# Kernel optimization log

Measured on AMD Instinct MI355X. Metric: run time of the kernel, lower is better.

## Reference

```python
import jax, jax.numpy as jnp
import numpy as np

H, KVH, D, BS, L = 32, 8, 128, 16, 4096
MAX_BLOCKS = L // BS          # 256 blocks per sequence (sink cache capacity)
B = 16
NUM_BLOCKS = B * MAX_BLOCKS   # 4096 total cache blocks
T = MAX_BLOCKS * BS           # 4096 linearized cache slots per sequence
SCALE = 1.0 / np.sqrt(D)


def _rope_cos_sin(pos):
    # neox-style RoPE tables; pos: int array [...]. returns cos/sin [..., D/2]
    inv_freq = 1.0 / (10000.0 ** (jnp.arange(0, D, 2, dtype=jnp.float32) / D))
    ang = pos[..., None].astype(jnp.float32) * inv_freq
    return jnp.cos(ang), jnp.sin(ang)


def _apply_rope(x, cos, sin):
    # x [..., D]; cos/sin broadcastable to x[..., :D//2]
    x1, x2 = jnp.split(x, 2, axis=-1)
    return jnp.concatenate([x1 * cos - x2 * sin, x2 * cos + x1 * sin], axis=-1)


def setup_inputs() -> dict:
    key = jax.random.key(0)
    ks = jax.random.split(key, 6)
    q = jax.random.normal(ks[0], (B, H * D), dtype=jnp.float32)
    k = jax.random.normal(ks[1], (B, KVH * D), dtype=jnp.float32)
    v = jax.random.normal(ks[2], (B, KVH * D), dtype=jnp.float32)
    key_cache = jax.random.normal(ks[3], (NUM_BLOCKS, BS, KVH, D), dtype=jnp.float32)
    value_cache = jax.random.normal(ks[4], (NUM_BLOCKS, BS, KVH, D), dtype=jnp.float32)
    block_tables = jnp.arange(B * MAX_BLOCKS, dtype=jnp.int32).reshape(B, MAX_BLOCKS)
    context_lens = jax.random.randint(ks[5], (B,), 0, 6000, dtype=jnp.int32)
    return {"q": q, "k": k, "v": v, "key_cache": key_cache,
            "value_cache": value_cache, "block_tables": block_tables,
            "context_lens": context_lens}


def reference(q, k, v, key_cache, value_cache, block_tables, context_lens):
    ctx = context_lens.astype(jnp.int32)                         # [B] past tokens
    rem = ctx % BS
    # sink/rolling cap: if past >= model_context_len, effective seq len caps
    seq_len = jnp.where(ctx >= L, L - BS + rem + 1, ctx + 1)     # [B]
    pos_q = seq_len - 1                                          # capped current position

    # gather pre-rope keys/values from paged cache -> [B, T, KVH, D]
    keys = key_cache[block_tables].reshape(B, T, KVH, D)
    vals = value_cache[block_tables].reshape(B, T, KVH, D)

    # re-apply rope to gathered keys at their cache-relative positions 0..T-1
    cos_k, sin_k = _rope_cos_sin(jnp.arange(T))                  # [T, D/2]
    keys = _apply_rope(keys, cos_k[None, :, None, :], sin_k[None, :, None, :])

    # rope current q, k at capped positions
    cos_q, sin_q = _rope_cos_sin(pos_q)                          # [B, D/2]
    qh = _apply_rope(q.reshape(B, H, D), cos_q[:, None, :], sin_q[:, None, :])
    kh = _apply_rope(k.reshape(B, KVH, D), cos_q[:, None, :], sin_q[:, None, :])

    # scatter current token's k/v at its slot (offset rem in last used block == seq_len-1)
    bidx = jnp.arange(B)
    keys = keys.at[bidx, pos_q].set(kh)
    vals = vals.at[bidx, pos_q].set(v.reshape(B, KVH, D))

    # GQA attention over first seq_len cached tokens
    G = H // KVH
    qg = qh.reshape(B, KVH, G, D)
    scores = jnp.einsum('bhgd,bthd->bhgt', qg, keys) * SCALE     # [B, KVH, G, T]
    mask = jnp.arange(T)[None, :] < seq_len[:, None]             # [B, T]
    scores = jnp.where(mask[:, None, None, :], scores, jnp.finfo(scores.dtype).min)
    probs = jax.nn.softmax(scores, axis=-1)
    out = jnp.einsum('bhgt,bthd->bhgd', probs, vals)             # [B, KVH, G, D]
    return out.reshape(B, H * D)
```

## Files before the change

kernel.cpp:

```cpp
#include <hip/hip_runtime.h>
#include <math.h>

#define B_      16
#define H_      32
#define KVH_    8
#define G_      4
#define D_      128
#define BS_     16
#define L_      4096
#define MAXB_   256
#define T_      4096
#define NPART_  8
#define PART_   512
#define SCALE_  0.08838834764831843f

__device__ __forceinline__ int seq_len_of(int ctx) {
  return (ctx >= L_) ? (L_ - BS_ + (ctx & (BS_ - 1)) + 1) : (ctx + 1);
}

__global__ void rope_table_kernel(float* __restrict__ tab) {
  int idx = blockIdx.x * blockDim.x + threadIdx.x;
  if (idx >= T_ * 64) return;
  int t = idx >> 6, i = idx & 63;
  double inv = pow(10000.0, -(double)(2 * i) / 128.0);
  float ang = (float)t * (float)inv;
  double a = (double)ang;
  tab[2 * idx]     = (float)cos(a);
  tab[2 * idx + 1] = (float)sin(a);
}

__global__ __launch_bounds__(256) void attn_partial_kernel(
    const float* __restrict__ q, const float* __restrict__ knew,
    const float* __restrict__ vnew, const float* __restrict__ kc,
    const float* __restrict__ vc, const int* __restrict__ btab,
    const int* __restrict__ ctxl, const float* __restrict__ tab,
    float* __restrict__ opart, float2* __restrict__ ml) {
  int bid  = blockIdx.x;
  int part = bid & (NPART_ - 1);
  int kvh  = (bid >> 3) & (KVH_ - 1);
  int b    = bid >> 6;

  int seq = seq_len_of(ctxl[b]);
  int t0 = part * PART_;
  if (t0 >= seq) return;
  int t1 = min(t0 + PART_, seq);
  int posq = seq - 1;

  int lane = threadIdx.x & 63;
  int wave = threadIdx.x >> 6;
  int tsub = lane >> 4;
  int dg   = lane & 15;

  const float4* tab4 = (const float4*)tab;
  float4 cq0 = tab4[posq * 32 + 2 * dg];
  float4 cq1 = tab4[posq * 32 + 2 * dg + 1];

  float q1[G_][4], q2[G_][4];
#pragma unroll
  for (int g = 0; g < G_; ++g) {
    const float* qp = q + b * (H_ * D_) + (kvh * G_ + g) * D_;
    float4 a  = *(const float4*)(qp + 4 * dg);
    float4 bq = *(const float4*)(qp + 64 + 4 * dg);
    q1[g][0] = (a.x * cq0.x - bq.x * cq0.y) * SCALE_;
    q2[g][0] = (bq.x * cq0.x + a.x * cq0.y) * SCALE_;
    q1[g][1] = (a.y * cq0.z - bq.y * cq0.w) * SCALE_;
    q2[g][1] = (bq.y * cq0.z + a.y * cq0.w) * SCALE_;
    q1[g][2] = (a.z * cq1.x - bq.z * cq1.y) * SCALE_;
    q2[g][2] = (bq.z * cq1.x + a.z * cq1.y) * SCALE_;
    q1[g][3] = (a.w * cq1.z - bq.w * cq1.w) * SCALE_;
    q2[g][3] = (bq.w * cq1.z + a.w * cq1.w) * SCALE_;
  }

  float kn1[4], kn2[4];
  float4 vna, vnb;
  {
    const float* kp = knew + b * (KVH_ * D_) + kvh * D_;
    float4 a  = *(const float4*)(kp + 4 * dg);
    float4 bq = *(const float4*)(kp + 64 + 4 * dg);
    kn1[0] = a.x * cq0.x - bq.x * cq0.y;  kn2[0] = bq.x * cq0.x + a.x * cq0.y;
    kn1[1] = a.y * cq0.z - bq.y * cq0.w;  kn2[1] = bq.y * cq0.z + a.y * cq0.w;
    kn1[2] = a.z * cq1.x - bq.z * cq1.y;  kn2[2] = bq.z * cq1.x + a.z * cq1.y;
    kn1[3] = a.w * cq1.z - bq.w * cq1.w;  kn2[3] = bq.w * cq1.z + a.w * cq1.w;
    const float* vp = vnew + b * (KVH_ * D_) + kvh * D_;
    vna = *(const float4*)(vp + 4 * dg);
    vnb = *(const float4*)(vp + 64 + 4 * dg);
  }

  float m[G_], l[G_], acc[G_][8];
#pragma unroll
  for (int g = 0; g < G_; ++g) {
    m[g] = -1e30f; l[g] = 0.f;
#pragma unroll
    for (int j = 0; j < 8; ++j) acc[g][j] = 0.f;
  }

  for (int tq = t0 + 4 * wave; tq < t1; tq += 16) {
    int t = tq + tsub;
    if (t < t1) {
      int blk  = btab[b * MAXB_ + (t >> 4)];
      int base = ((blk * BS_ + (t & (BS_ - 1))) * KVH_ + kvh) * D_;
      const float4* kc4 = (const float4*)(kc + base);
      const float4* vc4 = (const float4*)(vc + base);
      float4 ka = kc4[dg],      kb = kc4[16 + dg];
      float4 va = vc4[dg],      vb = vc4[16 + dg];
      float4 c0 = tab4[t * 32 + 2 * dg];
      float4 c1 = tab4[t * 32 + 2 * dg + 1];

      float kr1[4], kr2[4];
      kr1[0] = ka.x * c0.x - kb.x * c0.y;  kr2[0] = kb.x * c0.x + ka.x * c0.y;
      kr1[1] = ka.y * c0.z - kb.y * c0.w;  kr2[1] = kb.y * c0.z + ka.y * c0.w;
      kr1[2] = ka.z * c1.x - kb.z * c1.y;  kr2[2] = kb.z * c1.x + ka.z * c1.y;
      kr1[3] = ka.w * c1.z - kb.w * c1.w;  kr2[3] = kb.w * c1.z + ka.w * c1.w;
      if (t == posq) {
#pragma unroll
        for (int j = 0; j < 4; ++j) { kr1[j] = kn1[j]; kr2[j] = kn2[j]; }
        va = vna; vb = vnb;
      }

      float s[G_];
#pragma unroll
      for (int g = 0; g < G_; ++g) {
        s[g] = kr1[0] * q1[g][0] + kr2[0] * q2[g][0]
             + kr1[1] * q1[g][1] + kr2[1] * q2[g][1]
             + kr1[2] * q1[g][2] + kr2[2] * q2[g][2]
             + kr1[3] * q1[g][3] + kr2[3] * q2[g][3];
      }
#pragma unroll
      for (int off = 1; off <= 8; off <<= 1) {
#pragma unroll
        for (int g = 0; g < G_; ++g) s[g] += __shfl_xor(s[g], off);
      }
#pragma unroll
      for (int g = 0; g < G_; ++g) {
        float sv = s[g];
        float p;
        if (sv > m[g]) {
          float corr = __expf(m[g] - sv);
          l[g] *= corr;
#pragma unroll
          for (int j = 0; j < 8; ++j) acc[g][j] *= corr;
          m[g] = sv;
          p = 1.0f;
        } else {
          p = __expf(sv - m[g]);
        }
        l[g] += p;
        acc[g][0] += p * va.x; acc[g][1] += p * va.y;
        acc[g][2] += p * va.z; acc[g][3] += p * va.w;
        acc[g][4] += p * vb.x; acc[g][5] += p * vb.y;
        acc[g][6] += p * vb.z; acc[g][7] += p * vb.w;
      }
    }
  }

  auto merge_off = [&](int off) {
#pragma unroll
    for (int g = 0; g < G_; ++g) {
      float mo = __shfl_xor(m[g], off);
      float lo = __shfl_xor(l[g], off);
      float M  = fmaxf(m[g], mo);
      float fa = __expf(m[g] - M);
      float fb = __expf(mo - M);
      l[g] = l[g] * fa + lo * fb;
      m[g] = M;
#pragma unroll
      for (int j = 0; j < 8; ++j) {
        float ao = __shfl_xor(acc[g][j], off);
        acc[g][j] = acc[g][j] * fa + ao * fb;
      }
    }
  };
  merge_off(16);
  merge_off(32);

  __shared__ float  lds_acc[4][G_][D_];
  __shared__ float2 lds_ml[4][G_];
  if (lane < 16) {
#pragma unroll
    for (int g = 0; g < G_; ++g) {
#pragma unroll
      for (int j = 0; j < 8; ++j) {
        int dim = (j < 4) ? (4 * dg + j) : (64 + 4 * dg + (j - 4));
        lds_acc[wave][g][dim] = acc[g][j];
      }
      if (lane == 0) lds_ml[wave][g] = make_float2(m[g], l[g]);
    }
  }
  __syncthreads();
  if (wave == 0) {
    int w = tsub;
#pragma unroll
    for (int g = 0; g < G_; ++g) {
      float2 t2 = lds_ml[w][g];
      m[g] = t2.x; l[g] = t2.y;
#pragma unroll
      for (int j = 0; j < 8; ++j) {
        int dim = (j < 4) ? (4 * dg + j) : (64 + 4 * dg + (j - 4));
        acc[g][j] = lds_acc[w][g][dim];
      }
    }
    merge_off(16);
    merge_off(32);
    if (lane < 16) {
#pragma unroll
      for (int g = 0; g < G_; ++g) {
        float* op = opart + (size_t)(bid * G_ + g) * D_;
#pragma unroll
        for (int j = 0; j < 8; ++j) {
          int dim = (j < 4) ? (4 * dg + j) : (64 + 4 * dg + (j - 4));
          op[dim] = acc[g][j];
        }
        if (lane == 0) ml[bid * G_ + g] = make_float2(m[g], l[g]);
      }
    }
  }
}

__global__ void attn_reduce_kernel(const float* __restrict__ opart,
                                   const float2* __restrict__ ml,
                                   const int* __restrict__ ctxl,
                                   float* __restrict__ out) {
  int bh = blockIdx.x;
  int b = bh >> 5, h = bh & 31;
  int kvh = h >> 2, g = h & 3;
  int d = threadIdx.x;
  int seq = seq_len_of(ctxl[b]);
  int nlive = (seq + PART_ - 1) >> 9;
  int base = (b * KVH_ + kvh) * NPART_;

  float M = -1e30f;
  for (int p = 0; p < nlive; ++p) M = fmaxf(M, ml[(base + p) * G_ + g].x);
  float L = 0.f, O = 0.f;
  for (int p = 0; p < nlive; ++p) {
    float2 mlv = ml[(base + p) * G_ + g];
    float f = __expf(mlv.x - M);
    L += mlv.y * f;
    O += opart[(size_t)((base + p) * G_ + g) * D_ + d] * f;
  }
  out[b * (H_ * D_) + h * D_ + d] = O / L;
}

extern "C" void kernel_launch(void* const* d_in, const int* in_sizes, int n_in,
                              void* d_out, int out_size, void* d_ws, size_t ws_size,
                              hipStream_t stream) {
  const float* q    = (const float*)d_in[0];
  const float* k    = (const float*)d_in[1];
  const float* v    = (const float*)d_in[2];
  const float* kc   = (const float*)d_in[3];
  const float* vc   = (const float*)d_in[4];
  const int*   btab = (const int*)d_in[5];
  const int*   ctxl = (const int*)d_in[6];
  float* out = (float*)d_out;

  float*  tab   = (float*)d_ws;
  float*  opart = tab + (size_t)T_ * 64 * 2;
  float2* ml    = (float2*)(opart + (size_t)B_ * KVH_ * NPART_ * G_ * D_);

  rope_table_kernel<<<(T_ * 64 + 255) / 256, 256, 0, stream>>>(tab);
  attn_partial_kernel<<<B_ * KVH_ * NPART_, 256, 0, stream>>>(
      q, k, v, kc, vc, btab, ctxl, tab, opart, ml);
  attn_reduce_kernel<<<B_ * H_, D_, 0, stream>>>(opart, ml, ctxl, out);
}
```

Baseline: 143.0 us.

## Double-buffer KV loads, halve partition size, and stage block table in LDS

Splits the sequence into 16 partitions of 256 tokens instead of 8 of 512, which doubles the number of workgroups available to spread across compute units. Each wave's token loop is now software-pipelined with two register sets, so the next token's K/V and RoPE table loads are issued before the current token is processed. Block-table entries for the partition are staged once in shared memory, and the new-token K/V RoPE is computed lazily only on the matching slot. The cost is higher register pressure from the double buffer and more partial results for the reduce kernel to merge.

```diff
diff --git a/kernel.cpp b/kernel.cpp
--- a/kernel.cpp
+++ b/kernel.cpp
@@ -10,8 +10,8 @@
 #define L_      4096
 #define MAXB_   256
 #define T_      4096
-#define NPART_  8
-#define PART_   512
+#define NPART_  16
+#define PART_   256
 #define SCALE_  0.08838834764831843f
 
 __device__ __forceinline__ int seq_len_of(int ctx) {
@@ -29,6 +29,84 @@
   tab[2 * idx + 1] = (float)sin(a);
 }
 
+
+#define LOADK(P, tt)                                                        \
+  {                                                                         \
+    int blk_  = sblk[((tt) - t0) >> 4];                                     \
+    int base_ = ((blk_ * BS_ + ((tt) & (BS_ - 1))) * KVH_ + kvh) * D_;      \
+    const float4* kc4_ = (const float4*)(kc + base_);                       \
+    const float4* vc4_ = (const float4*)(vc + base_);                       \
+    P##ka = kc4_[dg];      P##kb = kc4_[16 + dg];                           \
+    P##va = vc4_[dg];      P##vb = vc4_[16 + dg];                           \
+    P##c0 = tab4[(tt) * 32 + 2 * dg];                                       \
+    P##c1 = tab4[(tt) * 32 + 2 * dg + 1];                                   \
+  }
+
+#define COMPUTE(P, tt)                                                      \
+  {                                                                         \
+    float kr1[4], kr2[4];                                                   \
+    kr1[0] = P##ka.x * P##c0.x - P##kb.x * P##c0.y;                         \
+    kr2[0] = P##kb.x * P##c0.x + P##ka.x * P##c0.y;                         \
+    kr1[1] = P##ka.y * P##c0.z - P##kb.y * P##c0.w;                         \
+    kr2[1] = P##kb.y * P##c0.z + P##ka.y * P##c0.w;                         \
+    kr1[2] = P##ka.z * P##c1.x - P##kb.z * P##c1.y;                         \
+    kr2[2] = P##kb.z * P##c1.x + P##ka.z * P##c1.y;                         \
+    kr1[3] = P##ka.w * P##c1.z - P##kb.w * P##c1.w;                         \
+    kr2[3] = P##kb.w * P##c1.z + P##ka.w * P##c1.w;                         \
+    float4 va_ = P##va, vb_ = P##vb;                                        \
+    if ((tt) == posq) {         \
+      const float* kp_ = knew + b * (KVH_ * D_) + kvh * D_;                 \
+      float4 a_  = *(const float4*)(kp_ + 4 * dg);                          \
+      float4 b_  = *(const float4*)(kp_ + 64 + 4 * dg);                     \
+      float4 q0_ = tab4[posq * 32 + 2 * dg];                                \
+      float4 q1_ = tab4[posq * 32 + 2 * dg + 1];                            \
+      kr1[0] = a_.x * q0_.x - b_.x * q0_.y;                                 \
+      kr2[0] = b_.x * q0_.x + a_.x * q0_.y;                                 \
+      kr1[1] = a_.y * q0_.z - b_.y * q0_.w;                                 \
+      kr2[1] = b_.y * q0_.z + a_.y * q0_.w;                                 \
+      kr1[2] = a_.z * q1_.x - b_.z * q1_.y;                                 \
+      kr2[2] = b_.z * q1_.x + a_.z * q1_.y;                                 \
+      kr1[3] = a_.w * q1_.z - b_.w * q1_.w;                                 \
+      kr2[3] = b_.w * q1_.z + a_.w * q1_.w;                                 \
+      const float* vp_ = vnew + b * (KVH_ * D_) + kvh * D_;                 \
+      va_ = *(const float4*)(vp_ + 4 * dg);                                 \
+      vb_ = *(const float4*)(vp_ + 64 + 4 * dg);                            \
+    }                                                                       \
+    float s[G_];                                                            \
+    _Pragma("unroll")                                                       \
+    for (int g = 0; g < G_; ++g) {                                          \
+      s[g] = kr1[0] * q1[g][0] + kr2[0] * q2[g][0]                          \
+           + kr1[1] * q1[g][1] + kr2[1] * q2[g][1]                          \
+           + kr1[2] * q1[g][2] + kr2[2] * q2[g][2]                          \
+           + kr1[3] * q1[g][3] + kr2[3] * q2[g][3];                         \
+    }                                                                       \
+    _Pragma("unroll")                                                       \
+    for (int off = 1; off <= 8; off <<= 1) {                                \
+      _Pragma("unroll")                                                     \
+      for (int g = 0; g < G_; ++g) s[g] += __shfl_xor(s[g], off);           \
+    }                                                                       \
+    _Pragma("unroll")                                                       \
+    for (int g = 0; g < G_; ++g) {                                          \
+      float sv = s[g];                                                      \
+      float p;                                                              \
+      if (sv > m[g]) {                                                      \
+        float corr = __expf(m[g] - sv);                                     \
+        l[g] *= corr;                                                       \
+        _Pragma("unroll")                                                   \
+        for (int j = 0; j < 8; ++j) acc[g][j] *= corr;                      \
+        m[g] = sv;                                                          \
+        p = 1.0f;                                                           \
+      } else {                                                              \
+        p = __expf(sv - m[g]);                                              \
+      }                                                                     \
+      l[g] += p;                                                            \
+      acc[g][0] += p * va_.x; acc[g][1] += p * va_.y;                       \
+      acc[g][2] += p * va_.z; acc[g][3] += p * va_.w;                       \
+      acc[g][4] += p * vb_.x; acc[g][5] += p * vb_.y;                       \
+      acc[g][6] += p * vb_.z; acc[g][7] += p * vb_.w;                       \
+    }                                                                       \
+  }
+
 __global__ __launch_bounds__(256) void attn_partial_kernel(
     const float* __restrict__ q, const float* __restrict__ knew,
     const float* __restrict__ vnew, const float* __restrict__ kc,
@@ -37,8 +115,8 @@
     float* __restrict__ opart, float2* __restrict__ ml) {
   int bid  = blockIdx.x;
   int part = bid & (NPART_ - 1);
-  int kvh  = (bid >> 3) & (KVH_ - 1);
-  int b    = bid >> 6;
+  int kvh  = (bid >> 4) & (KVH_ - 1);
+  int b    = bid >> 7;
 
   int seq = seq_len_of(ctxl[b]);
   int t0 = part * PART_;
@@ -51,39 +129,31 @@
   int tsub = lane >> 4;
   int dg   = lane & 15;
 
+  __shared__ int sblk[PART_ / BS_];
+  if (threadIdx.x < PART_ / BS_)
+    sblk[threadIdx.x] = btab[b * MAXB_ + (t0 >> 4) + threadIdx.x];
+  __syncthreads();
+
   const float4* tab4 = (const float4*)tab;
-  float4 cq0 = tab4[posq * 32 + 2 * dg];
-  float4 cq1 = tab4[posq * 32 + 2 * dg + 1];
 
   float q1[G_][4], q2[G_][4];
-#pragma unroll
-  for (int g = 0; g < G_; ++g) {
-    const float* qp = q + b * (H_ * D_) + (kvh * G_ + g) * D_;
-    float4 a  = *(const float4*)(qp + 4 * dg);
-    float4 bq = *(const float4*)(qp + 64 + 4 * dg);
-    q1[g][0] = (a.x * cq0.x - bq.x * cq0.y) * SCALE_;
-    q2[g][0] = (bq.x * cq0.x + a.x * cq0.y) * SCALE_;
-    q1[g][1] = (a.y * cq0.z - bq.y * cq0.w) * SCALE_;
-    q2[g][1] = (bq.y * cq0.z + a.y * cq0.w) * SCALE_;
-    q1[g][2] = (a.z * cq1.x - bq.z * cq1.y) * SCALE_;
-    q2[g][2] = (bq.z * cq1.x + a.z * cq1.y) * SCALE_;
-    q1[g][3] = (a.w * cq1.z - bq.w * cq1.w) * SCALE_;
-    q2[g][3] = (bq.w * cq1.z + a.w * cq1.w) * SCALE_;
-  }
-
-  float kn1[4], kn2[4];
-  float4 vna, vnb;
   {
-    const float* kp = knew + b * (KVH_ * D_) + kvh * D_;
-    float4 a  = *(const float4*)(kp + 4 * dg);
-    float4 bq = *(const float4*)(kp + 64 + 4 * dg);
-    kn1[0] = a.x * cq0.x - bq.x * cq0.y;  kn2[0] = bq.x * cq0.x + a.x * cq0.y;
-    kn1[1] = a.y * cq0.z - bq.y * cq0.w;  kn2[1] = bq.y * cq0.z + a.y * cq0.w;
-    kn1[2] = a.z * cq1.x - bq.z * cq1.y;  kn2[2] = bq.z * cq1.x + a.z * cq1.y;
-    kn1[3] = a.w * cq1.z - bq.w * cq1.w;  kn2[3] = bq.w * cq1.z + a.w * cq1.w;
-    const float* vp = vnew + b * (KVH_ * D_) + kvh * D_;
-    vna = *(const float4*)(vp + 4 * dg);
-    vnb = *(const float4*)(vp + 64 + 4 * dg);
+    float4 cq0 = tab4[posq * 32 + 2 * dg];
+    float4 cq1 = tab4[posq * 32 + 2 * dg + 1];
+#pragma unroll
+    for (int g = 0; g < G_; ++g) {
+      const float* qp = q + b * (H_ * D_) + (kvh * G_ + g) * D_;
+      float4 a  = *(const float4*)(qp + 4 * dg);
+      float4 bq = *(const float4*)(qp + 64 + 4 * dg);
+      q1[g][0] = (a.x * cq0.x - bq.x * cq0.y) * SCALE_;
+      q2[g][0] = (bq.x * cq0.x + a.x * cq0.y) * SCALE_;
+      q1[g][1] = (a.y * cq0.z - bq.y * cq0.w) * SCALE_;
+      q2[g][1] = (bq.y * cq0.z + a.y * cq0.w) * SCALE_;
+      q1[g][2] = (a.z * cq1.x - bq.z * cq1.y) * SCALE_;
+      q2[g][2] = (bq.z * cq1.x + a.z * cq1.y) * SCALE_;
+      q1[g][3] = (a.w * cq1.z - bq.w * cq1.w) * SCALE_;
+      q2[g][3] = (bq.w * cq1.z + a.w * cq1.w) * SCALE_;
+    }
   }
 
   float m[G_], l[G_], acc[G_][8];
@@ -94,61 +164,23 @@
     for (int j = 0; j < 8; ++j) acc[g][j] = 0.f;
   }
 
-  for (int tq = t0 + 4 * wave; tq < t1; tq += 16) {
-    int t = tq + tsub;
+  {
+    float4 Aka, Akb, Ava, Avb, Ac0, Ac1;
+    float4 Bka, Bkb, Bva, Bvb, Bc0, Bc1;
+    int t = t0 + 4 * wave + tsub;
     if (t < t1) {
-      int blk  = btab[b * MAXB_ + (t >> 4)];
-      int base = ((blk * BS_ + (t & (BS_ - 1))) * KVH_ + kvh) * D_;
-      const float4* kc4 = (const float4*)(kc + base);
-      const float4* vc4 = (const float4*)(vc + base);
-      float4 ka = kc4[dg],      kb = kc4[16 + dg];
-      float4 va = vc4[dg],      vb = vc4[16 + dg];
-      float4 c0 = tab4[t * 32 + 2 * dg];
-      float4 c1 = tab4[t * 32 + 2 * dg + 1];
-
-      float kr1[4], kr2[4];
-      kr1[0] = ka.x * c0.x - kb.x * c0.y;  kr2[0] = kb.x * c0.x + ka.x * c0.y;
-      kr1[1] = ka.y * c0.z - kb.y * c0.w;  kr2[1] = kb.y * c0.z + ka.y * c0.w;
-      kr1[2] = ka.z * c1.x - kb.z * c1.y;  kr2[2] = kb.z * c1.x + ka.z * c1.y;
-      kr1[3] = ka.w * c1.z - kb.w * c1.w;  kr2[3] = kb.w * c1.z + ka.w * c1.w;
-      if (t == posq) {
-#pragma unroll
-        for (int j = 0; j < 4; ++j) { kr1[j] = kn1[j]; kr2[j] = kn2[j]; }
-        va = vna; vb = vnb;
-      }
-
-      float s[G_];
-#pragma unroll
-      for (int g = 0; g < G_; ++g) {
-        s[g] = kr1[0] * q1[g][0] + kr2[0] * q2[g][0]
-             + kr1[1] * q1[g][1] + kr2[1] * q2[g][1]
-             + kr1[2] * q1[g][2] + kr2[2] * q2[g][2]
-             + kr1[3] * q1[g][3] + kr2[3] * q2[g][3];
-      }
-#pragma unroll
-      for (int off = 1; off <= 8; off <<= 1) {
-#pragma unroll
-        for (int g = 0; g < G_; ++g) s[g] += __shfl_xor(s[g], off);
-      }
-#pragma unroll
-      for (int g = 0; g < G_; ++g) {
-        float sv = s[g];
-        float p;
-        if (sv > m[g]) {
-          float corr = __expf(m[g] - sv);
-          l[g] *= corr;
-#pragma unroll
-          for (int j = 0; j < 8; ++j) acc[g][j] *= corr;
-          m[g] = sv;
-          p = 1.0f;
-        } else {
-          p = __expf(sv - m[g]);
-        }
-        l[g] += p;
-        acc[g][0] += p * va.x; acc[g][1] += p * va.y;
-        acc[g][2] += p * va.z; acc[g][3] += p * va.w;
-        acc[g][4] += p * vb.x; acc[g][5] += p * vb.y;
-        acc[g][6] += p * vb.z; acc[g][7] += p * vb.w;
+      LOADK(A, t);
+      while (1) {
+        int t2 = t + 16;
+        if (t2 < t1) LOADK(B, t2);
+        COMPUTE(A, t);
+        t = t2;
+        if (t >= t1) break;
+        t2 = t + 16;
+        if (t2 < t1) LOADK(A, t2);
+        COMPUTE(B, t);
+        t = t2;
+        if (t >= t1) break;
       }
     }
   }
@@ -225,7 +257,7 @@
   int kvh = h >> 2, g = h & 3;
   int d = threadIdx.x;
   int seq = seq_len_of(ctxl[b]);
-  int nlive = (seq + PART_ - 1) >> 9;
+  int nlive = (seq + PART_ - 1) / PART_;
   int base = (b * KVH_ + kvh) * NPART_;
 
   float M = -1e30f;
```

New measurement: 119.3 us. -16.6%, faster.
